# Kernel optimization log

Measured on AMD Instinct MI355X. Metric: run time of the kernel, lower is better.

Reference implementation:

```python
import jax, jax.numpy as jnp
import numpy as np

B, SQ, SK, D = 16, 2048, 2048, 64


def setup_inputs() -> dict:
    key = jax.random.key(0)
    kq, kk, kv, kl = jax.random.split(key, 4)
    queries = jax.random.normal(kq, (B, SQ, D), dtype=jnp.float32)
    keys = jax.random.normal(kk, (B, SK, D), dtype=jnp.float32)
    values = jax.random.normal(kv, (B, SK, D), dtype=jnp.float32)
    # per-batch valid key lengths in [1, SK]
    valid_lens = jax.random.randint(kl, (B,), 1, SK + 1)
    return {"queries": queries, "keys": keys, "values": values, "valid_lens": valid_lens}


def reference(queries, keys, values, valid_lens):
    d = queries.shape[-1]
    # scaled scores: [B, SQ, SK]
    scores = jnp.einsum('bqd,bkd->bqk', queries, keys) / jnp.sqrt(jnp.asarray(d, queries.dtype))
    # masked_softmax (d2l): positions >= valid_len get -1e6 before softmax
    key_pos = jnp.arange(scores.shape[-1])  # [SK]
    mask = key_pos[None, None, :] < valid_lens[:, None, None]  # [B,1,SK]
    scores = jnp.where(mask, scores, jnp.asarray(-1e6, scores.dtype))
    attn = jax.nn.softmax(scores, axis=-1)
    # dropout p=0.0 -> identity
    return jnp.einsum('bqk,bkd->bqd', attn, values)
```

## Files before the change

kernel.cpp:

```cpp
#include <hip/hip_runtime.h>

#define NB  16
#define SQn 2048
#define SKn 2048
#define DHn 64
#define KS  4

typedef float    f32x4 __attribute__((ext_vector_type(4)));
typedef _Float16 f16x8 __attribute__((ext_vector_type(8)));
typedef _Float16 f16x4 __attribute__((ext_vector_type(4)));

#define MFMA __builtin_amdgcn_mfma_f32_16x16x32_f16

__device__ __forceinline__ f16x8 cvt8(f32x4 a, f32x4 b) {
    f16x8 h;
    h[0] = (_Float16)a[0]; h[1] = (_Float16)a[1];
    h[2] = (_Float16)a[2]; h[3] = (_Float16)a[3];
    h[4] = (_Float16)b[0]; h[5] = (_Float16)b[1];
    h[6] = (_Float16)b[2]; h[7] = (_Float16)b[3];
    return h;
}

__device__ __forceinline__ void stage16(const void* g, unsigned char* base) {
    __builtin_amdgcn_global_load_lds(
        (const __attribute__((address_space(1))) unsigned int*)g,
        (__attribute__((address_space(3))) unsigned int*)base,
        16, 0, 0);
}

__global__ __launch_bounds__(256)
void prep_kernel(const float* __restrict__ Kg, const float* __restrict__ Vg,
                 _Float16* __restrict__ Kh, _Float16* __restrict__ VTh)
{
    const int tid = threadIdx.x;
    const int kt  = blockIdx.x;
    const int b   = blockIdx.y;
    const size_t tbase = ((size_t)b * SKn + (size_t)kt * 64) * DHn;

    {
        const float* s = Kg + tbase + tid * 16;
        f32x4 a0 = *(const f32x4*)(s);
        f32x4 a1 = *(const f32x4*)(s + 4);
        f32x4 a2 = *(const f32x4*)(s + 8);
        f32x4 a3 = *(const f32x4*)(s + 12);
        _Float16* d = Kh + tbase + tid * 16;
        *(f16x8*)d       = cvt8(a0, a1);
        *(f16x8*)(d + 8) = cvt8(a2, a3);
    }
    __shared__ float vt[64][68];
    {
        const int row = tid >> 2, cb = (tid & 3) * 16;
        const float* s = Vg + tbase + row * DHn + cb;
#pragma unroll
        for (int i = 0; i < 4; ++i)
            *(f32x4*)&vt[row][cb + 4 * i] = *(const f32x4*)(s + 4 * i);
    }
    __syncthreads();
    {
        const int d0 = tid >> 2, kc = (tid & 3) * 16;
        f16x8 o0, o1;
#pragma unroll
        for (int j = 0; j < 8; ++j) {
            o0[j] = (_Float16)vt[kc + j][d0];
            o1[j] = (_Float16)vt[kc + 8 + j][d0];
        }
        _Float16* d = VTh + ((size_t)b * DHn + d0) * SKn + (size_t)kt * 64 + kc;
        *(f16x8*)d       = o0;
        *(f16x8*)(d + 8) = o1;
    }
}

__global__ __launch_bounds__(256)
void attn_split(const float* __restrict__ Qg, const _Float16* __restrict__ Kh,
                const _Float16* __restrict__ VTh, const int* __restrict__ VL,
                float* __restrict__ Opart, float* __restrict__ lpart)
{
    const int tid   = threadIdx.x;
    const int wave  = tid >> 6;
    const int lane  = tid & 63;
    const int l15   = lane & 15;
    const int q4    = lane >> 4;
    const int qhalf = wave & 1;
    const int kpar  = wave >> 1;

    const int b  = blockIdx.x & 15;
    const int qb = (blockIdx.x >> 4) & 31;
    const int ks = blockIdx.x >> 9;

    const int vl     = VL[b];
    const int ntiles = (vl + 63) >> 6;
    if (ntiles <= ks) return;
    const int nrounds = ((ntiles - ks - 1) >> 3) + 1;

    __shared__ __align__(16) unsigned char smem[49152];
    unsigned char* Kt0 = smem;
    unsigned char* Kt1 = smem + 8192;
    unsigned char* Vt0 = smem + 16384;
    unsigned char* Vt1 = smem + 24576;
    unsigned char* Pb  = smem + 32768 + wave * 4096;
    float* mergeO = (float*)smem;
    float* mergeL = (float*)(smem + 32768);

    const float SCALE = 0.18033688011112042f;
    const int qbase = qb * 64 + qhalf * 32;

    f16x8 qf[2][2];
#pragma unroll
    for (int g = 0; g < 2; ++g) {
        const float* qrow = Qg + ((size_t)b * SQn + qbase + g * 16 + l15) * DHn + q4 * 8;
#pragma unroll
        for (int c = 0; c < 2; ++c) {
            f32x4 a  = *(const f32x4*)(qrow + c * 32);
            f32x4 a2 = *(const f32x4*)(qrow + c * 32 + 4);
            a *= SCALE; a2 *= SCALE;
            qf[g][c] = cvt8(a, a2);
        }
    }

    f32x4 O[2][4];
#pragma unroll
    for (int g = 0; g < 2; ++g)
#pragma unroll
        for (int t = 0; t < 4; ++t) O[g][t] = (f32x4){0.f, 0.f, 0.f, 0.f};
    float lacc[2] = {0.f, 0.f};

    const _Float16* KhB = Kh + (size_t)b * SKn * DHn;
    const _Float16* VTB = VTh + (size_t)b * DHn * SKn;

    const int slot0 = tid, slot1 = 256 + tid;
    const int row0 = slot0 >> 3, gl0 = (slot0 & 7) ^ (row0 & 7);
    const int row1 = slot1 >> 3, gl1 = (slot1 & 7) ^ (row1 & 7);
    const int lbase0 = (wave * 64) * 16;
    const int lbase1 = (256 + wave * 64) * 16;

    for (int r = 0; r < nrounds; ++r) {
        const int tileA = ks + 8 * r;
        const int tileB = tileA + 4;
        {
            const int ka = tileA * 64, kb = tileB * 64;
            stage16(KhB + (size_t)(ka + row0) * DHn + gl0 * 8, Kt0 + lbase0);
            stage16(KhB + (size_t)(ka + row1) * DHn + gl1 * 8, Kt0 + lbase1);
            stage16(KhB + (size_t)(kb + row0) * DHn + gl0 * 8, Kt1 + lbase0);
            stage16(KhB + (size_t)(kb + row1) * DHn + gl1 * 8, Kt1 + lbase1);
            stage16(VTB + (size_t)row0 * SKn + ka + gl0 * 8, Vt0 + lbase0);
            stage16(VTB + (size_t)row1 * SKn + ka + gl1 * 8, Vt0 + lbase1);
            stage16(VTB + (size_t)row0 * SKn + kb + gl0 * 8, Vt1 + lbase0);
            stage16(VTB + (size_t)row1 * SKn + kb + gl1 * 8, Vt1 + lbase1);
        }
        __syncthreads();

        const int kt = kpar ? tileB : tileA;
        if (kt < ntiles) {
            const unsigned char* Kb = kpar ? Kt1 : Kt0;
            const unsigned char* Vb = kpar ? Vt1 : Vt0;
            const int sw = l15 & 7;

            f32x4 st[2][4];
#pragma unroll
            for (int g = 0; g < 2; ++g)
#pragma unroll
                for (int t = 0; t < 4; ++t) st[g][t] = (f32x4){0.f, 0.f, 0.f, 0.f};
#pragma unroll
            for (int t = 0; t < 4; ++t) {
                const int row = 16 * t + l15;
#pragma unroll
                for (int c = 0; c < 2; ++c) {
                    f16x8 kf = *(const f16x8*)(Kb + row * 128 + ((((c << 2) | q4) ^ sw) * 16));
                    st[0][t] = MFMA(kf, qf[0][c], st[0][t], 0, 0, 0);
                    st[1][t] = MFMA(kf, qf[1][c], st[1][t], 0, 0, 0);
                }
            }

            const bool lastt = (kt == ntiles - 1) && (vl & 63);
#pragma unroll
            for (int g = 0; g < 2; ++g) {
                unsigned char* pdst = Pb + (g * 16 + l15) * 128 + (q4 & 1) * 8;
#pragma unroll
                for (int t = 0; t < 4; ++t) {
                    float p0 = __builtin_amdgcn_exp2f(st[g][t][0]);
                    float p1 = __builtin_amdgcn_exp2f(st[g][t][1]);
                    float p2 = __builtin_amdgcn_exp2f(st[g][t][2]);
                    float p3 = __builtin_amdgcn_exp2f(st[g][t][3]);
                    if (lastt) {
                        const int kb0 = kt * 64 + 16 * t + 4 * q4;
                        p0 = (kb0 + 0 < vl) ? p0 : 0.f;
                        p1 = (kb0 + 1 < vl) ? p1 : 0.f;
                        p2 = (kb0 + 2 < vl) ? p2 : 0.f;
                        p3 = (kb0 + 3 < vl) ? p3 : 0.f;
                    }
                    lacc[g] += (p0 + p1) + (p2 + p3);
                    f16x4 w;
                    w[0] = (_Float16)p0; w[1] = (_Float16)p1;
                    w[2] = (_Float16)p2; w[3] = (_Float16)p3;
                    *(f16x4*)(pdst + (((2 * t + (q4 >> 1)) ^ sw) * 16)) = w;
                }
            }
            asm volatile("" ::: "memory");

            f16x8 pf[2][2];
#pragma unroll
            for (int g = 0; g < 2; ++g) {
                const unsigned char* psrc = Pb + (g * 16 + l15) * 128;
                pf[g][0] = *(const f16x8*)(psrc + ((q4 ^ sw) * 16));
                pf[g][1] = *(const f16x8*)(psrc + (((4 | q4) ^ sw) * 16));
            }

#pragma unroll
            for (int t2 = 0; t2 < 4; ++t2) {
                const int row = 16 * t2 + l15;
#pragma unroll
                for (int c2 = 0; c2 < 2; ++c2) {
                    f16x8 vf = *(const f16x8*)(Vb + row * 128 + ((((c2 << 2) | q4) ^ sw) * 16));
                    O[0][t2] = MFMA(vf, pf[0][c2], O[0][t2], 0, 0, 0);
                    O[1][t2] = MFMA(vf, pf[1][c2], O[1][t2], 0, 0, 0);
                }
            }
        }
        __syncthreads();
    }

    if (kpar == 1) {
#pragma unroll
        for (int g = 0; g < 2; ++g) {
            const int x = g * 16 + l15;
#pragma unroll
            for (int t2 = 0; t2 < 4; ++t2) {
                const int gd = (4 * t2 + q4) ^ l15;
                *(f32x4*)((unsigned char*)mergeO + (qhalf * 32 + x) * 256 + gd * 16) = O[g][t2];
            }
            float lt = lacc[g];
            lt += __shfl_xor(lt, 16);
            lt += __shfl_xor(lt, 32);
            if (q4 == 0) mergeL[qhalf * 32 + x] = lt;
        }
    }
    __syncthreads();
    if (kpar == 0) {
        const size_t rowbase = (size_t)b * SQn + qbase;
#pragma unroll
        for (int g = 0; g < 2; ++g) {
            const int x = g * 16 + l15;
            float lt = lacc[g];
            lt += __shfl_xor(lt, 16);
            lt += __shfl_xor(lt, 32);
            lt += mergeL[qhalf * 32 + x];
            if (q4 == 0) lpart[(size_t)ks * (NB * SQn) + rowbase + x] = lt;
            float* orow = Opart + ((size_t)ks * (NB * SQn) + rowbase + x) * DHn;
#pragma unroll
            for (int t2 = 0; t2 < 4; ++t2) {
                const int gd = (4 * t2 + q4) ^ l15;
                f32x4 part = *(const f32x4*)((const unsigned char*)mergeO + (qhalf * 32 + x) * 256 + gd * 16);
                *(f32x4*)(orow + 16 * t2 + 4 * q4) = O[g][t2] + part;
            }
        }
    }
}

__global__ __launch_bounds__(256)
void merge_kernel(const float* __restrict__ Op, const float* __restrict__ lp,
                  const int* __restrict__ VL, float* __restrict__ Og)
{
    const int i   = blockIdx.x * 256 + threadIdx.x;
    const int row = i >> 4;
    const int dc  = (i & 15) * 4;
    const int b   = row >> 11;
    const int ntiles = (VL[b] + 63) >> 6;
    const int nact   = ntiles < KS ? ntiles : KS;

    f32x4 acc = (f32x4){0.f, 0.f, 0.f, 0.f};
    float l = 0.f;
    for (int s = 0; s < nact; ++s) {
        acc += *(const f32x4*)(Op + ((size_t)s * (NB * SQn) + row) * DHn + dc);
        l   += lp[(size_t)s * (NB * SQn) + row];
    }
    const float inv = 1.f / l;
    f32x4 r = acc;
    r *= inv;
    *(f32x4*)(Og + (size_t)row * DHn + dc) = r;
}

__global__ __launch_bounds__(256, 2)
void attn_fwd(const float* __restrict__ Qg, const float* __restrict__ Kg,
              const float* __restrict__ Vg, const int* __restrict__ VL,
              float* __restrict__ Og)
{
    const int tid  = threadIdx.x;
    const int wave = tid >> 6;
    const int lane = tid & 63;
    const int l15  = lane & 15;
    const int q4   = lane >> 4;
    const int b  = blockIdx.x & 15;
    const int qb = blockIdx.x >> 4;
    __shared__ __align__(16) unsigned char smemf[8192 + 8192 + 4 * 2048];
    unsigned char* Klds  = smemf;
    unsigned char* VTlds = smemf + 8192;
    unsigned char* Plds  = smemf + 16384 + wave * 2048;
    const int vl = VL[b];
    const int ntiles = (vl + 63) >> 6;
    const float SCALE = 0.18033688011112042f;
    f16x8 qfr[2];
    {
        const float* qrow = Qg + ((size_t)b * SQn + (size_t)qb * 64 + wave * 16 + l15) * DHn;
#pragma unroll
        for (int c = 0; c < 2; ++c) {
            const float* s = qrow + c * 32 + q4 * 8;
            f32x4 a = *(const f32x4*)s;
            f32x4 b2 = *(const f32x4*)(s + 4);
            a *= SCALE; b2 *= SCALE;
            qfr[c] = cvt8(a, b2);
        }
    }
    f32x4 O[4];
#pragma unroll
    for (int t = 0; t < 4; ++t) O[t] = (f32x4){0.f, 0.f, 0.f, 0.f};
    float m_i[4] = {-3e38f, -3e38f, -3e38f, -3e38f};
    float l_i[4] = {0.f, 0.f, 0.f, 0.f};
    for (int kt = 0; kt < ntiles; ++kt) {
        const int k0 = kt * 64;
#pragma unroll
        for (int i = 0; i < 2; ++i) {
            int g8 = tid + i * 256;
            int row = g8 >> 3, g = g8 & 7;
            const float* s = Kg + ((size_t)b * SKn + k0 + row) * DHn + g * 8;
            f32x4 a = *(const f32x4*)s;
            f32x4 c4 = *(const f32x4*)(s + 4);
            *(f16x8*)(Klds + row * 128 + ((g ^ (row & 7)) * 16)) = cvt8(a, c4);
        }
        {
            int key = tid & 63, dg = tid >> 6;
            const float* s = Vg + ((size_t)b * SKn + k0 + key) * DHn + dg * 16;
            int swz = key >> 3;
            int koff = (key & 7) * 2;
#pragma unroll
            for (int i = 0; i < 4; ++i) {
                f32x4 v4 = *(const f32x4*)(s + i * 4);
#pragma unroll
                for (int j = 0; j < 4; ++j) {
                    int d = dg * 16 + i * 4 + j;
                    *(_Float16*)(VTlds + d * 128 + ((swz ^ (d & 7)) * 16) + koff) = (_Float16)v4[j];
                }
            }
        }
        __syncthreads();
        f32x4 accs[4];
#pragma unroll
        for (int t = 0; t < 4; ++t) accs[t] = (f32x4){0.f, 0.f, 0.f, 0.f};
#pragma unroll
        for (int t = 0; t < 4; ++t) {
            int row = t * 16 + l15;
#pragma unroll
            for (int c = 0; c < 2; ++c) {
                f16x8 kf = *(const f16x8*)(Klds + row * 128 + ((((c << 2) + q4) ^ (l15 & 7)) * 16));
                accs[t] = MFMA(qfr[c], kf, accs[t], 0, 0, 0);
            }
        }
        if (k0 + 64 > vl) {
#pragma unroll
            for (int t = 0; t < 4; ++t)
                if (k0 + t * 16 + l15 >= vl) accs[t] = (f32x4){-1e30f, -1e30f, -1e30f, -1e30f};
        }
        float al[4];
#pragma unroll
        for (int rr = 0; rr < 4; ++rr) {
            float v = fmaxf(fmaxf(accs[0][rr], accs[1][rr]), fmaxf(accs[2][rr], accs[3][rr]));
            v = fmaxf(v, __shfl_xor(v, 1));
            v = fmaxf(v, __shfl_xor(v, 2));
            v = fmaxf(v, __shfl_xor(v, 4));
            v = fmaxf(v, __shfl_xor(v, 8));
            float mnew = fmaxf(m_i[rr], v);
            al[rr] = __builtin_amdgcn_exp2f(m_i[rr] - mnew);
            m_i[rr] = mnew;
        }
#pragma unroll
        for (int rr = 0; rr < 4; ++rr) {
            float s0 = 0.f;
#pragma unroll
            for (int t = 0; t < 4; ++t) {
                float p = __builtin_amdgcn_exp2f(accs[t][rr] - m_i[rr]);
                accs[t][rr] = p;
                s0 += p;
            }
            s0 += __shfl_xor(s0, 1);
            s0 += __shfl_xor(s0, 2);
            s0 += __shfl_xor(s0, 4);
            s0 += __shfl_xor(s0, 8);
            l_i[rr] = l_i[rr] * al[rr] + s0;
            O[0][rr] *= al[rr]; O[1][rr] *= al[rr]; O[2][rr] *= al[rr]; O[3][rr] *= al[rr];
        }
#pragma unroll
        for (int rr = 0; rr < 4; ++rr) {
            int row = q4 * 4 + rr;
            int swz = row & 7;
#pragma unroll
            for (int t = 0; t < 4; ++t) {
                int g = t * 2 + (l15 >> 3);
                *(_Float16*)(Plds + row * 128 + ((g ^ swz) * 16) + (l15 & 7) * 2) = (_Float16)accs[t][rr];
            }
        }
        asm volatile("" ::: "memory");
        f16x8 pfr[2];
        pfr[0] = *(const f16x8*)(Plds + l15 * 128 + ((q4 ^ (l15 & 7)) * 16));
        pfr[1] = *(const f16x8*)(Plds + l15 * 128 + (((4 + q4) ^ (l15 & 7)) * 16));
#pragma unroll
        for (int t2 = 0; t2 < 4; ++t2) {
            int d = t2 * 16 + l15;
#pragma unroll
            for (int c2 = 0; c2 < 2; ++c2) {
                f16x8 vf = *(const f16x8*)(VTlds + d * 128 + ((((c2 << 2) + q4) ^ (l15 & 7)) * 16));
                O[t2] = MFMA(pfr[c2], vf, O[t2], 0, 0, 0);
            }
        }
        __syncthreads();
    }
    float inv[4];
#pragma unroll
    for (int rr = 0; rr < 4; ++rr) inv[rr] = 1.f / l_i[rr];
    float* orow = Og + ((size_t)b * SQn + (size_t)qb * 64 + wave * 16 + q4 * 4) * DHn;
#pragma unroll
    for (int rr = 0; rr < 4; ++rr)
#pragma unroll
        for (int t2 = 0; t2 < 4; ++t2)
            orow[rr * DHn + t2 * 16 + l15] = O[t2][rr] * inv[rr];
}

extern "C" void kernel_launch(void* const* d_in, const int* in_sizes, int n_in,
                              void* d_out, int out_size, void* d_ws, size_t ws_size,
                              hipStream_t stream) {
    (void)in_sizes; (void)n_in; (void)out_size;
    const float* Q = (const float*)d_in[0];
    const float* K = (const float*)d_in[1];
    const float* V = (const float*)d_in[2];
    const int*  VLp = (const int*)d_in[3];
    float* O = (float*)d_out;

    const size_t kv_elems = (size_t)NB * SKn * DHn;
    const size_t rows     = (size_t)NB * SQn;
    const size_t off_Kh = 0;
    const size_t off_VT = kv_elems * sizeof(_Float16);
    const size_t off_Op = off_VT + kv_elems * sizeof(_Float16);
    const size_t off_lp = off_Op + (size_t)KS * rows * DHn * sizeof(float);
    const size_t need   = off_lp + (size_t)KS * rows * sizeof(float);

    if (ws_size >= need) {
        _Float16* Kh  = (_Float16*)((char*)d_ws + off_Kh);
        _Float16* VTh = (_Float16*)((char*)d_ws + off_VT);
        float* Opart  = (float*)((char*)d_ws + off_Op);
        float* lpart  = (float*)((char*)d_ws + off_lp);
        hipLaunchKernelGGL(prep_kernel, dim3(SKn / 64, NB), dim3(256), 0, stream, K, V, Kh, VTh);
        hipLaunchKernelGGL(attn_split, dim3(NB * (SQn / 64) * KS), dim3(256), 0, stream,
                           Q, Kh, VTh, VLp, Opart, lpart);
        hipLaunchKernelGGL(merge_kernel, dim3((NB * SQn * DHn / 4) / 256), dim3(256), 0, stream,
                           Opart, lpart, VLp, O);
    } else {
        hipLaunchKernelGGL(attn_fwd, dim3(NB * (SQn / 64)), dim3(256), 0, stream, Q, K, V, VLp, O);
    }
}
```

Before: 117.5 us.

## Restructure split-K attention: waves own query tiles, read K/V directly, fp16 partials

The split-K attention kernel is rewritten so each of the four waves owns its own 32 query rows. Each wave loads K and V^T fragments straight from global memory into registers, replacing the shared-memory staging with global_load_lds and the block-wide barriers. The row sum is now computed with an MFMA against a ones vector instead of scalar adds and shuffles, and fp16 conversions use packed cvt_pkrtz. Partial outputs are stored as fp16 to halve the intermediate traffic read by the merge kernel. The cost is more redundant global and L2 reads, since K/V are no longer shared across waves through LDS, and some loss of precision in the partials.

```diff
diff --git a/kernel.cpp b/kernel.cpp
--- a/kernel.cpp
+++ b/kernel.cpp
@@ -9,23 +9,31 @@
 typedef float    f32x4 __attribute__((ext_vector_type(4)));
 typedef _Float16 f16x8 __attribute__((ext_vector_type(8)));
 typedef _Float16 f16x4 __attribute__((ext_vector_type(4)));
+typedef _Float16 f16x2 __attribute__((ext_vector_type(2)));
+typedef __fp16   fp16x2 __attribute__((ext_vector_type(2)));
 
 #define MFMA __builtin_amdgcn_mfma_f32_16x16x32_f16
 
+union H8 { f16x8 v; f16x2 h[4]; };
+union H4 { f16x4 v; f16x2 h[2]; };
+
+__device__ __forceinline__ f16x2 pk(float a, float b) {
+    fp16x2 r = __builtin_amdgcn_cvt_pkrtz(a, b);
+    return __builtin_bit_cast(f16x2, r);
+}
+
+__device__ __forceinline__ f16x8 pack8(float a0, float a1, float a2, float a3,
+                                       float a4, float a5, float a6, float a7) {
+    H8 u;
+    u.h[0] = pk(a0, a1);
+    u.h[1] = pk(a2, a3);
+    u.h[2] = pk(a4, a5);
+    u.h[3] = pk(a6, a7);
+    return u.v;
+}
+
 __device__ __forceinline__ f16x8 cvt8(f32x4 a, f32x4 b) {
-    f16x8 h;
-    h[0] = (_Float16)a[0]; h[1] = (_Float16)a[1];
-    h[2] = (_Float16)a[2]; h[3] = (_Float16)a[3];
-    h[4] = (_Float16)b[0]; h[5] = (_Float16)b[1];
-    h[6] = (_Float16)b[2]; h[7] = (_Float16)b[3];
-    return h;
-}
-
-__device__ __forceinline__ void stage16(const void* g, unsigned char* base) {
-    __builtin_amdgcn_global_load_lds(
-        (const __attribute__((address_space(1))) unsigned int*)g,
-        (__attribute__((address_space(3))) unsigned int*)base,
-        16, 0, 0);
+    return pack8(a[0], a[1], a[2], a[3], b[0], b[1], b[2], b[3]);
 }
 
 __global__ __launch_bounds__(256)
@@ -71,38 +79,30 @@
 }
 
 __global__ __launch_bounds__(256)
-void attn_split(const float* __restrict__ Qg, const _Float16* __restrict__ Kh,
-                const _Float16* __restrict__ VTh, const int* __restrict__ VL,
-                float* __restrict__ Opart, float* __restrict__ lpart)
+void attn_ws(const float* __restrict__ Qg, const _Float16* __restrict__ Kh,
+             const _Float16* __restrict__ VTh, const int* __restrict__ VL,
+             _Float16* __restrict__ Opart, float* __restrict__ lpart)
 {
-    const int tid   = threadIdx.x;
-    const int wave  = tid >> 6;
-    const int lane  = tid & 63;
-    const int l15   = lane & 15;
-    const int q4    = lane >> 4;
-    const int qhalf = wave & 1;
-    const int kpar  = wave >> 1;
+    const int tid  = threadIdx.x;
+    const int wave = tid >> 6;
+    const int lane = tid & 63;
+    const int l15  = lane & 15;
+    const int q4   = lane >> 4;
 
     const int b  = blockIdx.x & 15;
-    const int qb = (blockIdx.x >> 4) & 31;
-    const int ks = blockIdx.x >> 9;
+    const int ks = (blockIdx.x >> 4) & 3;
+    const int gq = ((blockIdx.x >> 6) << 2) | wave;
 
     const int vl     = VL[b];
     const int ntiles = (vl + 63) >> 6;
     if (ntiles <= ks) return;
-    const int nrounds = ((ntiles - ks - 1) >> 3) + 1;
-
-    __shared__ __align__(16) unsigned char smem[49152];
-    unsigned char* Kt0 = smem;
-    unsigned char* Kt1 = smem + 8192;
-    unsigned char* Vt0 = smem + 16384;
-    unsigned char* Vt1 = smem + 24576;
-    unsigned char* Pb  = smem + 32768 + wave * 4096;
-    float* mergeO = (float*)smem;
-    float* mergeL = (float*)(smem + 32768);
+
+    __shared__ __align__(16) unsigned char smem[16384];
+    unsigned char* Pb = smem + wave * 4096;
+    const int sw = l15 & 7;
 
     const float SCALE = 0.18033688011112042f;
-    const int qbase = qb * 64 + qhalf * 32;
+    const int qbase = gq * 32;
 
     f16x8 qf[2][2];
 #pragma unroll
@@ -110,154 +110,124 @@
         const float* qrow = Qg + ((size_t)b * SQn + qbase + g * 16 + l15) * DHn + q4 * 8;
 #pragma unroll
         for (int c = 0; c < 2; ++c) {
-            f32x4 a  = *(const f32x4*)(qrow + c * 32);
-            f32x4 a2 = *(const f32x4*)(qrow + c * 32 + 4);
-            a *= SCALE; a2 *= SCALE;
-            qf[g][c] = cvt8(a, a2);
-        }
-    }
+            f32x4 x = *(const f32x4*)(qrow + c * 32);
+            f32x4 y = *(const f32x4*)(qrow + c * 32 + 4);
+            qf[g][c] = pack8(x[0] * SCALE, x[1] * SCALE, x[2] * SCALE, x[3] * SCALE,
+                             y[0] * SCALE, y[1] * SCALE, y[2] * SCALE, y[3] * SCALE);
+        }
+    }
+
+    f16x8 ones;
+#pragma unroll
+    for (int j = 0; j < 8; ++j) ones[j] = (_Float16)1.0f;
 
     f32x4 O[2][4];
 #pragma unroll
     for (int g = 0; g < 2; ++g)
 #pragma unroll
         for (int t = 0; t < 4; ++t) O[g][t] = (f32x4){0.f, 0.f, 0.f, 0.f};
-    float lacc[2] = {0.f, 0.f};
-
-    const _Float16* KhB = Kh + (size_t)b * SKn * DHn;
-    const _Float16* VTB = VTh + (size_t)b * DHn * SKn;
-
-    const int slot0 = tid, slot1 = 256 + tid;
-    const int row0 = slot0 >> 3, gl0 = (slot0 & 7) ^ (row0 & 7);
-    const int row1 = slot1 >> 3, gl1 = (slot1 & 7) ^ (row1 & 7);
-    const int lbase0 = (wave * 64) * 16;
-    const int lbase1 = (256 + wave * 64) * 16;
-
-    for (int r = 0; r < nrounds; ++r) {
-        const int tileA = ks + 8 * r;
-        const int tileB = tileA + 4;
-        {
-            const int ka = tileA * 64, kb = tileB * 64;
-            stage16(KhB + (size_t)(ka + row0) * DHn + gl0 * 8, Kt0 + lbase0);
-            stage16(KhB + (size_t)(ka + row1) * DHn + gl1 * 8, Kt0 + lbase1);
-            stage16(KhB + (size_t)(kb + row0) * DHn + gl0 * 8, Kt1 + lbase0);
-            stage16(KhB + (size_t)(kb + row1) * DHn + gl1 * 8, Kt1 + lbase1);
-            stage16(VTB + (size_t)row0 * SKn + ka + gl0 * 8, Vt0 + lbase0);
-            stage16(VTB + (size_t)row1 * SKn + ka + gl1 * 8, Vt0 + lbase1);
-            stage16(VTB + (size_t)row0 * SKn + kb + gl0 * 8, Vt1 + lbase0);
-            stage16(VTB + (size_t)row1 * SKn + kb + gl1 * 8, Vt1 + lbase1);
-        }
-        __syncthreads();
-
-        const int kt = kpar ? tileB : tileA;
-        if (kt < ntiles) {
-            const unsigned char* Kb = kpar ? Kt1 : Kt0;
-            const unsigned char* Vb = kpar ? Vt1 : Vt0;
-            const int sw = l15 & 7;
-
-            f32x4 st[2][4];
-#pragma unroll
-            for (int g = 0; g < 2; ++g)
-#pragma unroll
-                for (int t = 0; t < 4; ++t) st[g][t] = (f32x4){0.f, 0.f, 0.f, 0.f};
+    f32x4 lC[2];
+    lC[0] = (f32x4){0.f, 0.f, 0.f, 0.f};
+    lC[1] = (f32x4){0.f, 0.f, 0.f, 0.f};
+
+    const _Float16* Kp  = Kh + ((size_t)b * SKn + (size_t)ks * 64) * DHn;
+    const _Float16* VTb = VTh + (size_t)b * DHn * SKn + (size_t)ks * 64;
+
+    for (int kt = ks; kt < ntiles; kt += KS) {
+        const _Float16* Kt = Kp + (size_t)(kt - ks) * DHn * 64;
+        const _Float16* Vt = VTb + (size_t)(kt - ks) * 64;
+
+        f16x8 kf[4][2];
+#pragma unroll
+        for (int t = 0; t < 4; ++t)
+#pragma unroll
+            for (int c = 0; c < 2; ++c)
+                kf[t][c] = *(const f16x8*)(Kt + (16 * t + l15) * DHn + c * 32 + q4 * 8);
+
+        f16x8 vf[4][2];
+#pragma unroll
+        for (int t2 = 0; t2 < 4; ++t2)
+#pragma unroll
+            for (int c2 = 0; c2 < 2; ++c2)
+                vf[t2][c2] = *(const f16x8*)(Vt + (size_t)(16 * t2 + l15) * SKn + c2 * 32 + q4 * 8);
+
+        f32x4 st[2][4];
+#pragma unroll
+        for (int g = 0; g < 2; ++g)
+#pragma unroll
+            for (int t = 0; t < 4; ++t) st[g][t] = (f32x4){0.f, 0.f, 0.f, 0.f};
+#pragma unroll
+        for (int t = 0; t < 4; ++t)
+#pragma unroll
+            for (int c = 0; c < 2; ++c) {
+                st[0][t] = MFMA(kf[t][c], qf[0][c], st[0][t], 0, 0, 0);
+                st[1][t] = MFMA(kf[t][c], qf[1][c], st[1][t], 0, 0, 0);
+            }
+
+        const bool lastt = (kt == ntiles - 1) && (vl & 63);
+#pragma unroll
+        for (int g = 0; g < 2; ++g) {
+            unsigned char* pdst = Pb + (g * 16 + l15) * 128 + (q4 & 1) * 8;
 #pragma unroll
             for (int t = 0; t < 4; ++t) {
-                const int row = 16 * t + l15;
-#pragma unroll
-                for (int c = 0; c < 2; ++c) {
-                    f16x8 kf = *(const f16x8*)(Kb + row * 128 + ((((c << 2) | q4) ^ sw) * 16));
-                    st[0][t] = MFMA(kf, qf[0][c], st[0][t], 0, 0, 0);
-                    st[1][t] = MFMA(kf, qf[1][c], st[1][t], 0, 0, 0);
+                float p0 = __builtin_amdgcn_exp2f(st[g][t][0]);
+                float p1 = __builtin_amdgcn_exp2f(st[g][t][1]);
+                float p2 = __builtin_amdgcn_exp2f(st[g][t][2]);
+                float p3 = __builtin_amdgcn_exp2f(st[g][t][3]);
+                if (lastt) {
+                    const int kb0 = kt * 64 + 16 * t + 4 * q4;
+                    p0 = (kb0 + 0 < vl) ? p0 : 0.f;
+                    p1 = (kb0 + 1 < vl) ? p1 : 0.f;
+                    p2 = (kb0 + 2 < vl) ? p2 : 0.f;
+                    p3 = (kb0 + 3 < vl) ? p3 : 0.f;
                 }
-            }
-
-            const bool lastt = (kt == ntiles - 1) && (vl & 63);
-#pragma unroll
-            for (int g = 0; g < 2; ++g) {
-                unsigned char* pdst = Pb + (g * 16 + l15) * 128 + (q4 & 1) * 8;
-#pragma unroll
-                for (int t = 0; t < 4; ++t) {
-                    float p0 = __builtin_amdgcn_exp2f(st[g][t][0]);
-                    float p1 = __builtin_amdgcn_exp2f(st[g][t][1]);
-                    float p2 = __builtin_amdgcn_exp2f(st[g][t][2]);
-                    float p3 = __builtin_amdgcn_exp2f(st[g][t][3]);
-                    if (lastt) {
-                        const int kb0 = kt * 64 + 16 * t + 4 * q4;
-                        p0 = (kb0 + 0 < vl) ? p0 : 0.f;
-                        p1 = (kb0 + 1 < vl) ? p1 : 0.f;
-                        p2 = (kb0 + 2 < vl) ? p2 : 0.f;
-                        p3 = (kb0 + 3 < vl) ? p3 : 0.f;
-                    }
-                    lacc[g] += (p0 + p1) + (p2 + p3);
-                    f16x4 w;
-                    w[0] = (_Float16)p0; w[1] = (_Float16)p1;
-                    w[2] = (_Float16)p2; w[3] = (_Float16)p3;
-                    *(f16x4*)(pdst + (((2 * t + (q4 >> 1)) ^ sw) * 16)) = w;
-                }
-            }
-            asm volatile("" ::: "memory");
-
-            f16x8 pf[2][2];
-#pragma unroll
-            for (int g = 0; g < 2; ++g) {
-                const unsigned char* psrc = Pb + (g * 16 + l15) * 128;
-                pf[g][0] = *(const f16x8*)(psrc + ((q4 ^ sw) * 16));
-                pf[g][1] = *(const f16x8*)(psrc + (((4 | q4) ^ sw) * 16));
-            }
-
-#pragma unroll
-            for (int t2 = 0; t2 < 4; ++t2) {
-                const int row = 16 * t2 + l15;
-#pragma unroll
-                for (int c2 = 0; c2 < 2; ++c2) {
-                    f16x8 vf = *(const f16x8*)(Vb + row * 128 + ((((c2 << 2) | q4) ^ sw) * 16));
-                    O[0][t2] = MFMA(vf, pf[0][c2], O[0][t2], 0, 0, 0);
-                    O[1][t2] = MFMA(vf, pf[1][c2], O[1][t2], 0, 0, 0);
-                }
-            }
-        }
-        __syncthreads();
-    }
-
-    if (kpar == 1) {
+                H4 w;
+                w.h[0] = pk(p0, p1);
+                w.h[1] = pk(p2, p3);
+                *(f16x4*)(pdst + (((2 * t + (q4 >> 1)) ^ sw) * 16)) = w.v;
+            }
+        }
+        asm volatile("" ::: "memory");
+
+        f16x8 pf[2][2];
 #pragma unroll
         for (int g = 0; g < 2; ++g) {
-            const int x = g * 16 + l15;
-#pragma unroll
-            for (int t2 = 0; t2 < 4; ++t2) {
-                const int gd = (4 * t2 + q4) ^ l15;
-                *(f32x4*)((unsigned char*)mergeO + (qhalf * 32 + x) * 256 + gd * 16) = O[g][t2];
-            }
-            float lt = lacc[g];
-            lt += __shfl_xor(lt, 16);
-            lt += __shfl_xor(lt, 32);
-            if (q4 == 0) mergeL[qhalf * 32 + x] = lt;
-        }
-    }
-    __syncthreads();
-    if (kpar == 0) {
-        const size_t rowbase = (size_t)b * SQn + qbase;
-#pragma unroll
-        for (int g = 0; g < 2; ++g) {
-            const int x = g * 16 + l15;
-            float lt = lacc[g];
-            lt += __shfl_xor(lt, 16);
-            lt += __shfl_xor(lt, 32);
-            lt += mergeL[qhalf * 32 + x];
-            if (q4 == 0) lpart[(size_t)ks * (NB * SQn) + rowbase + x] = lt;
-            float* orow = Opart + ((size_t)ks * (NB * SQn) + rowbase + x) * DHn;
-#pragma unroll
-            for (int t2 = 0; t2 < 4; ++t2) {
-                const int gd = (4 * t2 + q4) ^ l15;
-                f32x4 part = *(const f32x4*)((const unsigned char*)mergeO + (qhalf * 32 + x) * 256 + gd * 16);
-                *(f32x4*)(orow + 16 * t2 + 4 * q4) = O[g][t2] + part;
-            }
+            const unsigned char* psrc = Pb + (g * 16 + l15) * 128;
+            pf[g][0] = *(const f16x8*)(psrc + ((q4 ^ sw) * 16));
+            pf[g][1] = *(const f16x8*)(psrc + (((4 | q4) ^ sw) * 16));
+        }
+
+#pragma unroll
+        for (int t2 = 0; t2 < 4; ++t2)
+#pragma unroll
+            for (int c2 = 0; c2 < 2; ++c2) {
+                O[0][t2] = MFMA(vf[t2][c2], pf[0][c2], O[0][t2], 0, 0, 0);
+                O[1][t2] = MFMA(vf[t2][c2], pf[1][c2], O[1][t2], 0, 0, 0);
+            }
+#pragma unroll
+        for (int c2 = 0; c2 < 2; ++c2) {
+            lC[0] = MFMA(ones, pf[0][c2], lC[0], 0, 0, 0);
+            lC[1] = MFMA(ones, pf[1][c2], lC[1], 0, 0, 0);
+        }
+    }
+
+#pragma unroll
+    for (int g = 0; g < 2; ++g) {
+        const size_t qrow = (size_t)ks * (NB * SQn) + (size_t)b * SQn + qbase + g * 16 + l15;
+        if (q4 == 0) lpart[qrow] = lC[g][0];
+        _Float16* od = Opart + qrow * DHn;
+#pragma unroll
+        for (int t2 = 0; t2 < 4; ++t2) {
+            H4 w;
+            w.h[0] = pk(O[g][t2][0], O[g][t2][1]);
+            w.h[1] = pk(O[g][t2][2], O[g][t2][3]);
+            *(f16x4*)(od + 16 * t2 + 4 * q4) = w.v;
         }
     }
 }
 
 __global__ __launch_bounds__(256)
-void merge_kernel(const float* __restrict__ Op, const float* __restrict__ lp,
+void merge_kernel(const _Float16* __restrict__ Op, const float* __restrict__ lp,
                   const int* __restrict__ VL, float* __restrict__ Og)
 {
     const int i   = blockIdx.x * 256 + threadIdx.x;
@@ -270,13 +240,14 @@
     f32x4 acc = (f32x4){0.f, 0.f, 0.f, 0.f};
     float l = 0.f;
     for (int s = 0; s < nact; ++s) {
-        acc += *(const f32x4*)(Op + ((size_t)s * (NB * SQn) + row) * DHn + dc);
-        l   += lp[(size_t)s * (NB * SQn) + row];
+        f16x4 h = *(const f16x4*)(Op + ((size_t)s * (NB * SQn) + row) * DHn + dc);
+        acc[0] += (float)h[0]; acc[1] += (float)h[1];
+        acc[2] += (float)h[2]; acc[3] += (float)h[3];
+        l += lp[(size_t)s * (NB * SQn) + row];
     }
     const float inv = 1.f / l;
-    f32x4 r = acc;
-    r *= inv;
-    *(f32x4*)(Og + (size_t)row * DHn + dc) = r;
+    acc *= inv;
+    *(f32x4*)(Og + (size_t)row * DHn + dc) = acc;
 }
 
 __global__ __launch_bounds__(256, 2)
@@ -438,16 +409,16 @@
     const size_t off_Kh = 0;
     const size_t off_VT = kv_elems * sizeof(_Float16);
     const size_t off_Op = off_VT + kv_elems * sizeof(_Float16);
-    const size_t off_lp = off_Op + (size_t)KS * rows * DHn * sizeof(float);
+    const size_t off_lp = off_Op + (size_t)KS * rows * DHn * sizeof(_Float16);
     const size_t need   = off_lp + (size_t)KS * rows * sizeof(float);
 
     if (ws_size >= need) {
-        _Float16* Kh  = (_Float16*)((char*)d_ws + off_Kh);
-        _Float16* VTh = (_Float16*)((char*)d_ws + off_VT);
-        float* Opart  = (float*)((char*)d_ws + off_Op);
-        float* lpart  = (float*)((char*)d_ws + off_lp);
+        _Float16* Kh    = (_Float16*)((char*)d_ws + off_Kh);
+        _Float16* VTh   = (_Float16*)((char*)d_ws + off_VT);
+        _Float16* Opart = (_Float16*)((char*)d_ws + off_Op);
+        float* lpart    = (float*)((char*)d_ws + off_lp);
         hipLaunchKernelGGL(prep_kernel, dim3(SKn / 64, NB), dim3(256), 0, stream, K, V, Kh, VTh);
-        hipLaunchKernelGGL(attn_split, dim3(NB * (SQn / 64) * KS), dim3(256), 0, stream,
+        hipLaunchKernelGGL(attn_ws, dim3(NB * KS * (SQn / 128)), dim3(256), 0, stream,
                            Q, Kh, VTh, VLp, Opart, lpart);
         hipLaunchKernelGGL(merge_kernel, dim3((NB * SQn * DHn / 4) / 256), dim3(256), 0, stream,
                            Opart, lpart, VLp, O);
```

Result: slower. 142.9 us (+21.6%).
